# Kernel optimization log

Hardware: AMD Instinct MI355X
Metric: run time of the kernel (lower is better)

## Reference

```python
import jax, jax.numpy as jnp
import numpy as np

TAU_PRE = 2.0
TAU_POST = 2.0


def setup_inputs() -> dict:
    key = jax.random.key(0)
    k1, k2, k3 = jax.random.split(key, 3)
    T, B, PRE, POST = 64, 16, 4096, 4096
    in_spikes = jax.random.uniform(k1, (T, B, PRE), dtype=jnp.float32)
    out_spikes = jax.random.uniform(k2, (T, B, POST), dtype=jnp.float32)
    weight = jax.random.normal(k3, (POST, PRE), dtype=jnp.float32)
    return {"in_spikes": in_spikes, "out_spikes": out_spikes, "weight": weight}


def reference(in_spikes, out_spikes, weight):
    # in_spikes: [T, B, pre]; out_spikes: [T, B, post]; weight: [post, pre]
    T, B, PRE = in_spikes.shape
    POST = out_spikes.shape[-1]

    def step(carry, xs):
        trace_pre, trace_post, delta_w = carry
        i_sp, o_sp = xs
        trace_pre = jnp.clip(trace_pre - trace_pre / TAU_PRE + i_sp, 0.0, 1.0)  # [B, pre]
        trace_post = trace_post - trace_post / TAU_POST + o_sp  # [B, post]
        # sum_b o[b,post]*trace_pre[b,pre] - (sum_b o[b,post]*trace_post[b,post]) * w[post,pre]
        dw = (jnp.einsum('bo,bp->op', o_sp, trace_pre)
              - (o_sp * trace_post).sum(0)[:, None] * weight)
        return (trace_pre, trace_post, delta_w + dw), None

    init = (jnp.zeros((B, PRE), in_spikes.dtype),
            jnp.zeros((B, POST), out_spikes.dtype),
            jnp.zeros((POST, PRE), weight.dtype))
    (trace_pre, trace_post, delta_w), _ = jax.lax.scan(step, init, (in_spikes, out_spikes))
    return delta_w
```

## Files before the change

kernel.cpp:

```cpp
#include <hip/hip_runtime.h>


#define T_STEPS 64
#define B_SZ    16
#define PRE     4096
#define POST    4096
#define K_TOT   1024

typedef __attribute__((ext_vector_type(8))) unsigned short ushort8;
typedef __attribute__((ext_vector_type(8))) __bf16 bf16x8;
typedef __attribute__((ext_vector_type(4))) float floatx4;

__device__ __forceinline__ unsigned short f2bf(float f) {
    unsigned int u = __float_as_uint(f);
    u += 0x7fff + ((u >> 16) & 1);
    return (unsigned short)(u >> 16);
}

__global__ __launch_bounds__(256) void trace_pre_bt(const float* __restrict__ in_spikes,
                                                    unsigned short* __restrict__ BT) {
    __shared__ unsigned short tile[16][K_TOT];
    const int tid = threadIdx.x;
    const int b  = tid >> 4;
    const int xl = tid & 15;
    const int x0 = blockIdx.x * 16;
    const float* src = in_spikes + (size_t)b * PRE + (x0 + xl);
    float tp = 0.f;
    #pragma unroll 8
    for (int t = 0; t < T_STEPS; ++t) {
        float x = src[(size_t)t * (B_SZ * PRE)];
        tp = 0.5f * tp + x;
        tp = fminf(fmaxf(tp, 0.f), 1.f);
        tile[xl][(t * 16 + b + xl * 8) & (K_TOT - 1)] = f2bf(tp);
    }
    __syncthreads();
    const int row = tid >> 4;
    const int c0  = tid & 15;
    #pragma unroll
    for (int i = 0; i < 8; ++i) {
        int ch = c0 + i * 16;
        ushort8 v = *(const ushort8*)&tile[row][((ch + row) & 127) * 8];
        *(ushort8*)&BT[(size_t)(x0 + row) * K_TOT + ch * 8] = v;
    }
}

__global__ __launch_bounds__(256) void conv_o_at(const float* __restrict__ out_spikes,
                                                 unsigned short* __restrict__ AT,
                                                 float* __restrict__ coef) {
    __shared__ unsigned short tile[16][K_TOT];
    __shared__ float cbuf[16][17];
    const int tid = threadIdx.x;
    const int b  = tid >> 4;
    const int xl = tid & 15;
    const int x0 = blockIdx.x * 16;
    const float* src = out_spikes + (size_t)b * POST + (x0 + xl);
    float po = 0.f, c = 0.f;
    #pragma unroll 8
    for (int t = 0; t < T_STEPS; ++t) {
        float x = src[(size_t)t * (B_SZ * POST)];
        po = 0.5f * po + x;
        c += x * po;
        tile[xl][(t * 16 + b + xl * 8) & (K_TOT - 1)] = f2bf(x);
    }
    cbuf[b][xl] = c;
    __syncthreads();
    if (tid < 16) {
        float s = 0.f;
        #pragma unroll
        for (int bb = 0; bb < 16; ++bb) s += cbuf[bb][tid];
        coef[x0 + tid] = s;
    }
    const int row = tid >> 4;
    const int c0  = tid & 15;
    #pragma unroll
    for (int i = 0; i < 8; ++i) {
        int ch = c0 + i * 16;
        ushort8 v = *(const ushort8*)&tile[row][((ch + row) & 127) * 8];
        *(ushort8*)&AT[(size_t)(x0 + row) * K_TOT + ch * 8] = v;
    }
}

#define BM 128
#define BN 128
#define BK 32

__device__ __forceinline__ void glds16(const void* g, void* l) {
    __builtin_amdgcn_global_load_lds((const __attribute__((address_space(1))) void*)g,
                                     (__attribute__((address_space(3))) void*)l,
                                     16, 0, 0);
}

__global__ __launch_bounds__(256) void stdp_gemm_mfma(
        const unsigned short* __restrict__ AT,
        const unsigned short* __restrict__ BT,
        const float* __restrict__ W,
        const float* __restrict__ coef,
        float* __restrict__ Cout) {
    __shared__ unsigned short As[BM][BK];
    __shared__ unsigned short Bs[BN][BK];
    const int tid  = threadIdx.x;
    const int lane = tid & 63;
    const int wave = tid >> 6;
    const int wm = (wave >> 1) * 64;
    const int wn = (wave & 1) * 64;
    const int m0 = blockIdx.y * BM;
    const int n0 = blockIdx.x * BN;

    floatx4 acc[4][4];
    #pragma unroll
    for (int i = 0; i < 4; ++i)
        #pragma unroll
        for (int j = 0; j < 4; ++j)
            acc[i][j] = (floatx4){0.f, 0.f, 0.f, 0.f};

    const int srow = tid >> 2;
    const int sk   = (tid & 3) * 8;
    const unsigned short* ga = &AT[(size_t)(m0 + srow) * K_TOT + sk];
    const unsigned short* gb = &BT[(size_t)(n0 + srow) * K_TOT + sk];
    unsigned short* la = &As[0][0] + (tid >> 6) * 512;
    unsigned short* lb = &Bs[0][0] + (tid >> 6) * 512;

    const int rm = lane & 15;
    const int kq = (lane >> 4) * 8;

    for (int k0 = 0; k0 < K_TOT; k0 += BK) {
        glds16(ga,              la);
        glds16(ga + 64 * K_TOT, la + 64 * BK);
        glds16(gb,              lb);
        glds16(gb + 64 * K_TOT, lb + 64 * BK);
        ga += BK; gb += BK;
        __syncthreads();

        bf16x8 af[4], bv[4];
        #pragma unroll
        for (int i = 0; i < 4; ++i) {
            af[i] = *(const bf16x8*)&As[wm + i * 16 + rm][kq];
            bv[i] = *(const bf16x8*)&Bs[wn + i * 16 + rm][kq];
        }
        #pragma unroll
        for (int mi = 0; mi < 4; ++mi)
            #pragma unroll
            for (int ni = 0; ni < 4; ++ni)
                acc[mi][ni] = __builtin_amdgcn_mfma_f32_16x16x32_bf16(
                    af[mi], bv[ni], acc[mi][ni], 0, 0, 0);
        __syncthreads();
    }

    const int colp = n0 + wn + rm;
    const int rowb = m0 + wm + (lane >> 4) * 4;
    #pragma unroll
    for (int mi = 0; mi < 4; ++mi) {
        #pragma unroll
        for (int r = 0; r < 4; ++r) {
            const int o = rowb + mi * 16 + r;
            const float cf = coef[o];
            const float* wr = &W[(size_t)o * PRE];
            float* cr = &Cout[(size_t)o * PRE];
            #pragma unroll
            for (int ni = 0; ni < 4; ++ni) {
                const int p = colp + ni * 16;
                cr[p] = acc[mi][ni][r] - cf * wr[p];
            }
        }
    }
}

extern "C" void kernel_launch(void* const* d_in, const int* in_sizes, int n_in,
                              void* d_out, int out_size, void* d_ws, size_t ws_size,
                              hipStream_t stream) {
    const float* in_spikes  = (const float*)d_in[0];
    const float* out_spikes = (const float*)d_in[1];
    const float* weight     = (const float*)d_in[2];
    float* out = (float*)d_out;

    unsigned short* AT = (unsigned short*)d_ws;
    unsigned short* BT = AT + (size_t)POST * K_TOT;
    float* coef = (float*)(BT + (size_t)PRE * K_TOT);

    trace_pre_bt<<<PRE  / 16, 256, 0, stream>>>(in_spikes, BT);
    conv_o_at  <<<POST / 16, 256, 0, stream>>>(out_spikes, AT, coef);

    dim3 grid(PRE / BN, POST / BM);
    stdp_gemm_mfma<<<grid, 256, 0, stream>>>(AT, BT, weight, coef, out);
}
```

Before: 193.4 us.

## Merge trace preprocessing kernels and XOR-swizzle GEMM LDS tiles

Merges the two preprocessing kernels (pre-trace to BT, out-spike to AT plus coefficient) into one 512-block launch, with each thread batching 16 timestep loads before running the recurrence. The GEMM's global-to-LDS loads now place each row's 16-byte k-chunk at an XOR-swizzled position, and the fragment reads use the matching swizzle, to reduce LDS bank conflicts. This saves one launch and gives more memory-level parallelism, at the cost of a divergent branch per block and more registers for the batched loads.

```diff
diff --git a/kernel.cpp b/kernel.cpp
--- a/kernel.cpp
+++ b/kernel.cpp
@@ -17,54 +17,48 @@
     return (unsigned short)(u >> 16);
 }
 
-__global__ __launch_bounds__(256) void trace_pre_bt(const float* __restrict__ in_spikes,
-                                                    unsigned short* __restrict__ BT) {
-    __shared__ unsigned short tile[16][K_TOT];
-    const int tid = threadIdx.x;
-    const int b  = tid >> 4;
-    const int xl = tid & 15;
-    const int x0 = blockIdx.x * 16;
-    const float* src = in_spikes + (size_t)b * PRE + (x0 + xl);
-    float tp = 0.f;
-    #pragma unroll 8
-    for (int t = 0; t < T_STEPS; ++t) {
-        float x = src[(size_t)t * (B_SZ * PRE)];
-        tp = 0.5f * tp + x;
-        tp = fminf(fmaxf(tp, 0.f), 1.f);
-        tile[xl][(t * 16 + b + xl * 8) & (K_TOT - 1)] = f2bf(tp);
-    }
-    __syncthreads();
-    const int row = tid >> 4;
-    const int c0  = tid & 15;
-    #pragma unroll
-    for (int i = 0; i < 8; ++i) {
-        int ch = c0 + i * 16;
-        ushort8 v = *(const ushort8*)&tile[row][((ch + row) & 127) * 8];
-        *(ushort8*)&BT[(size_t)(x0 + row) * K_TOT + ch * 8] = v;
-    }
-}
-
-__global__ __launch_bounds__(256) void conv_o_at(const float* __restrict__ out_spikes,
-                                                 unsigned short* __restrict__ AT,
-                                                 float* __restrict__ coef) {
+__global__ __launch_bounds__(256) void trace_convert(
+        const float* __restrict__ in_spikes,
+        const float* __restrict__ out_spikes,
+        unsigned short* __restrict__ AT,
+        unsigned short* __restrict__ BT,
+        float* __restrict__ coef) {
     __shared__ unsigned short tile[16][K_TOT];
     __shared__ float cbuf[16][17];
     const int tid = threadIdx.x;
     const int b  = tid >> 4;
     const int xl = tid & 15;
-    const int x0 = blockIdx.x * 16;
-    const float* src = out_spikes + (size_t)b * POST + (x0 + xl);
-    float po = 0.f, c = 0.f;
-    #pragma unroll 8
-    for (int t = 0; t < T_STEPS; ++t) {
-        float x = src[(size_t)t * (B_SZ * POST)];
-        po = 0.5f * po + x;
-        c += x * po;
-        tile[xl][(t * 16 + b + xl * 8) & (K_TOT - 1)] = f2bf(x);
+    const bool isA = blockIdx.x >= 256;
+    const int x0 = (isA ? blockIdx.x - 256 : blockIdx.x) * 16;
+    const float* src = (isA ? out_spikes : in_spikes) + (size_t)b * 4096 + x0 + xl;
+    unsigned short* dst = isA ? AT : BT;
+
+    float state = 0.f, c = 0.f;
+    for (int tc = 0; tc < 4; ++tc) {
+        float xs[16];
+        #pragma unroll
+        for (int j = 0; j < 16; ++j)
+            xs[j] = src[(size_t)(tc * 16 + j) * (B_SZ * PRE)];
+        if (isA) {
+            #pragma unroll
+            for (int j = 0; j < 16; ++j) {
+                const int t = tc * 16 + j;
+                state = 0.5f * state + xs[j];
+                c += xs[j] * state;
+                tile[xl][(t * 16 + b + xl * 8) & (K_TOT - 1)] = f2bf(xs[j]);
+            }
+        } else {
+            #pragma unroll
+            for (int j = 0; j < 16; ++j) {
+                const int t = tc * 16 + j;
+                state = fminf(fmaxf(0.5f * state + xs[j], 0.f), 1.f);
+                tile[xl][(t * 16 + b + xl * 8) & (K_TOT - 1)] = f2bf(state);
+            }
+        }
     }
-    cbuf[b][xl] = c;
+    if (isA) cbuf[b][xl] = c;
     __syncthreads();
-    if (tid < 16) {
+    if (isA && tid < 16) {
         float s = 0.f;
         #pragma unroll
         for (int bb = 0; bb < 16; ++bb) s += cbuf[bb][tid];
@@ -74,9 +68,9 @@
     const int c0  = tid & 15;
     #pragma unroll
     for (int i = 0; i < 8; ++i) {
-        int ch = c0 + i * 16;
+        const int ch = c0 + i * 16;
         ushort8 v = *(const ushort8*)&tile[row][((ch + row) & 127) * 8];
-        *(ushort8*)&AT[(size_t)(x0 + row) * K_TOT + ch * 8] = v;
+        *(ushort8*)&dst[(size_t)(x0 + row) * K_TOT + ch * 8] = v;
     }
 }
 
@@ -114,14 +108,15 @@
             acc[i][j] = (floatx4){0.f, 0.f, 0.f, 0.f};
 
     const int srow = tid >> 2;
-    const int sk   = (tid & 3) * 8;
-    const unsigned short* ga = &AT[(size_t)(m0 + srow) * K_TOT + sk];
-    const unsigned short* gb = &BT[(size_t)(n0 + srow) * K_TOT + sk];
-    unsigned short* la = &As[0][0] + (tid >> 6) * 512;
-    unsigned short* lb = &Bs[0][0] + (tid >> 6) * 512;
+    const int qg   = (tid & 3) ^ ((srow >> 1) & 3);
+    const unsigned short* ga = &AT[(size_t)(m0 + srow) * K_TOT + qg * 8];
+    const unsigned short* gb = &BT[(size_t)(n0 + srow) * K_TOT + qg * 8];
+    unsigned short* la = &As[0][0] + wave * 512;
+    unsigned short* lb = &Bs[0][0] + wave * 512;
 
-    const int rm = lane & 15;
-    const int kq = (lane >> 4) * 8;
+    const int rm  = lane & 15;
+    const int q   = lane >> 4;
+    const int kqs = (q ^ ((rm >> 1) & 3)) * 8;
 
     for (int k0 = 0; k0 < K_TOT; k0 += BK) {
         glds16(ga,              la);
@@ -134,8 +129,8 @@
         bf16x8 af[4], bv[4];
         #pragma unroll
         for (int i = 0; i < 4; ++i) {
-            af[i] = *(const bf16x8*)&As[wm + i * 16 + rm][kq];
-            bv[i] = *(const bf16x8*)&Bs[wn + i * 16 + rm][kq];
+            af[i] = *(const bf16x8*)&As[wm + i * 16 + rm][kqs];
+            bv[i] = *(const bf16x8*)&Bs[wn + i * 16 + rm][kqs];
         }
         #pragma unroll
         for (int mi = 0; mi < 4; ++mi)
@@ -177,8 +172,7 @@
     unsigned short* BT = AT + (size_t)POST * K_TOT;
     float* coef = (float*)(BT + (size_t)PRE * K_TOT);
 
-    trace_pre_bt<<<PRE  / 16, 256, 0, stream>>>(in_spikes, BT);
-    conv_o_at  <<<POST / 16, 256, 0, stream>>>(out_spikes, AT, coef);
+    trace_convert<<<512, 256, 0, stream>>>(in_spikes, out_spikes, AT, BT, coef);
 
     dim3 grid(PRE / BN, POST / BM);
     stdp_gemm_mfma<<<grid, 256, 0, stream>>>(AT, BT, weight, coef, out);
```

Result: no change. 191.3 us (-1.1%).
